# Kernel optimization log

Measured on AMD Instinct MI355X. Metric: run time of the kernel, lower is better.

Reference implementation:

```python
import jax, jax.numpy as jnp
import numpy as np
from jax import lax

F8 = jnp.float8_e4m3fn


def setup_inputs() -> dict:
    key = jax.random.key(0)
    kx, kw = jax.random.split(key)
    x = jax.random.normal(kx, (2, 128, 4, 192, 320), dtype=jnp.float32)
    # matches reset_parameters: normal(0, 0.02) then cast to fp8
    weight = jax.random.normal(kw, (128, 128, 3, 3, 3), dtype=jnp.float32) * 0.02
    return {"x": x, "weight": weight}


def reference(x, weight):
    # fp8 e4m3 quantization round-trip (the torch module stores/consumes fp8),
    # compute/accumulate in fp32 as an fp8 conv kernel would.
    xq = x.astype(F8).astype(jnp.float32)
    wq = weight.astype(F8).astype(jnp.float32)
    # causal temporal padding: (kT-1, 0) = (2, 0); spatial 'same' padding (1,1)
    xp = jnp.pad(xq, ((0, 0), (0, 0), (2, 0), (1, 1), (1, 1)))
    out = lax.conv_general_dilated(
        xp, wq,
        window_strides=(1, 1, 1),
        padding='VALID',
        dimension_numbers=('NCDHW', 'OIDHW', 'NCDHW'),
    )  # (B, 128, 4, 192, 320)
    return out
```

## Files before the change

kernel.cpp:

```cpp
#include <hip/hip_runtime.h>
#include <hip/hip_fp8.h>


using f32x16 = __attribute__((ext_vector_type(16))) float;
using i32x8 = __attribute__((ext_vector_type(8))) int;
typedef long long i64;
struct alignas(16) L2v { i64 x, y; };

namespace {
constexpr int Cc = 128, Dd = 4, Hh = 192, Ww = 320;
constexpr int HP = 194, WP = 322;
constexpr int NTAP = 27;
constexpr size_t PLANE = (size_t)4 * WP * 32;
constexpr size_t XQ_BYTES = (size_t)2 * Dd * HP * PLANE;
constexpr int ZA = 8 * 2 * 2576;
constexpr int ZB = 8 * 192 * 32;
constexpr int GSTR = WP * 32;
}

__global__ __launch_bounds__(256) void zero_pad_kernel(unsigned char* __restrict__ xq) {
  int i = blockIdx.x * 256 + threadIdx.x;
  if (i < ZA) {
    int bd = i / (2 * 2576);
    int r = i - bd * (2 * 2576);
    int hsel = r / 2576, seg = r - hsel * 2576;
    L2v z{0, 0};
    *(L2v*)(xq + ((size_t)bd * HP + (hsel ? 193 : 0)) * PLANE + (size_t)seg * 16) = z;
  } else if (i < ZA + ZB) {
    int j = i - ZA;
    int bd = j / (192 * 32);
    int r = j - bd * (192 * 32);
    int h = r / 32 + 1;
    int t = r & 31;
    int g = t >> 3, s2 = t & 7;
    int wsel = s2 >> 2, part = s2 & 3;
    *(i64*)(xq + ((size_t)bd * HP + h) * PLANE + (size_t)g * GSTR
            + (size_t)(wsel ? 321 : 0) * 32 + part * 8) = 0;
  }
}

__global__ __launch_bounds__(256) void qx_kernel(const float* __restrict__ x,
                                                 unsigned char* __restrict__ xq) {
  __shared__ unsigned char lt[64 * 136];
  const int tid = threadIdx.x;
  const int b = blockIdx.z >> 2, d = blockIdx.z & 3;
  const int h = blockIdx.y;
  const int w0 = blockIdx.x * 64;
  const int wl = tid & 63, cig = tid >> 6;
  const size_t cstr = (size_t)Dd * Hh * Ww;
  const float* xp = x + (((size_t)b * Cc * Dd + d) * Hh + h) * Ww + w0 + wl;
  #pragma unroll 4
  for (int i = 0; i < 32; ++i) {
    int ci = cig * 32 + i;
    __hip_fp8_e4m3 q(xp[ci * cstr]);
    lt[wl * 136 + ci] = q.__x;
  }
  __syncthreads();
  unsigned char* plane = xq + ((size_t)(b * Dd + d) * HP + h + 1) * PLANE;
  {
    int g = tid >> 6, w = tid & 63;
    const unsigned char* src = lt + w * 136 + g * 32;
    i64 a0 = *(const i64*)(src), a1 = *(const i64*)(src + 8);
    i64 a2 = *(const i64*)(src + 16), a3 = *(const i64*)(src + 24);
    unsigned char* dst = plane + (size_t)g * GSTR + (size_t)(w0 + 1 + w) * 32;
    *(L2v*)dst = L2v{a0, a1};
    *(L2v*)(dst + 16) = L2v{a2, a3};
  }
}

__global__ void wpack_kernel(const float* __restrict__ w, unsigned char* __restrict__ wpk) {
  int idx = blockIdx.x * 256 + threadIdx.x;
  if (idx >= Cc * Cc * NTAP) return;
  int tap = idx % NTAP;
  int t = idx / NTAP;
  int ci = t % Cc, co = t / Cc;
  int cc = ci >> 6, ct = co >> 5;
  int lane = (((ci >> 5) & 1) << 5) | (co & 31);
  __hip_fp8_e4m3 q(w[idx]);
  wpk[((((size_t)tap * 2 + cc) * 4 + ct) * 64 + lane) * 32 + (ci & 31)] = q.__x;
}

__global__ __launch_bounds__(256, 3) void conv_mfma(const unsigned char* __restrict__ xq,
                                                    const unsigned char* __restrict__ wpk,
                                                    float* __restrict__ out) {
  __shared__ unsigned char lb[24 * 2112];
  const int tid = threadIdx.x;
  const int lane = tid & 63, wv = tid >> 6;
  const int l31 = lane & 31, chalf = lane >> 5;
  const int hr = wv >> 1, ch = wv & 1;
  const int b = blockIdx.z >> 2, dout = blockIdx.z & 3;
  const int h0 = blockIdx.y * 2;
  const int w0 = blockIdx.x * 64;
  const int kdmin = dout >= 2 ? 0 : 2 - dout;

  f32x16 acc[2][2];
  #pragma unroll
  for (int a = 0; a < 2; ++a)
    #pragma unroll
    for (int n = 0; n < 2; ++n)
      #pragma unroll
      for (int r = 0; r < 16; ++r) acc[a][n][r] = 0.f;

  for (int cc = 0; cc < 2; ++cc) {
    __syncthreads();
    for (int u = tid + kdmin * 528; u < 1584; u += 256) {
      int w = u % 66;
      int rest = u / 66;
      int chf = rest & 1, rest2 = rest >> 1;
      int hrow = rest2 & 3, kd = rest2 >> 2;
      const unsigned char* src = xq
          + ((size_t)(b * Dd + dout + kd - 2) * HP + h0 + hrow) * PLANE
          + (size_t)(cc * 2 + chf) * GSTR + (size_t)(w0 + w) * 32;
      L2v lo = *(const L2v*)src;
      L2v hi = *(const L2v*)(src + 16);
      int t = (w >> 2) & 1;
      unsigned char* base = lb + rest * 2112;
      *(L2v*)(base + (2 * w + t) * 16) = lo;
      *(L2v*)(base + (2 * w + 1 - t) * 16) = hi;
    }
    __syncthreads();
    __builtin_amdgcn_s_setprio(1);
    for (int kd = kdmin; kd < 3; ++kd) {
      #pragma unroll
      for (int kh = 0; kh < 3; ++kh) {
        i32x8 av[3][2];
        #pragma unroll
        for (int kw = 0; kw < 3; ++kw)
          #pragma unroll
          for (int ct = 0; ct < 2; ++ct) {
            const unsigned char* ap = wpk +
                ((((size_t)(kd * 9 + kh * 3 + kw) * 2 + cc) * 4 + ch * 2 + ct) * 64 + lane) * 32;
            int4 alo = *(const int4*)ap;
            int4 ahi = *(const int4*)(ap + 16);
            av[kw][ct][0] = alo.x; av[kw][ct][1] = alo.y;
            av[kw][ct][2] = alo.z; av[kw][ct][3] = alo.w;
            av[kw][ct][4] = ahi.x; av[kw][ct][5] = ahi.y;
            av[kw][ct][6] = ahi.z; av[kw][ct][7] = ahi.w;
          }
        const unsigned char* pbase = lb + (((kd * 4 + hr + kh) * 2 + chalf)) * 2112;
        #pragma unroll
        for (int kw = 0; kw < 3; ++kw)
          #pragma unroll
          for (int nf = 0; nf < 2; ++nf) {
            int wl = nf * 32 + l31 + kw;
            int t = (wl >> 2) & 1;
            int4 blo = *(const int4*)(pbase + (2 * wl + t) * 16);
            int4 bhi = *(const int4*)(pbase + (2 * wl + 1 - t) * 16);
            i32x8 bv;
            bv[0] = blo.x; bv[1] = blo.y; bv[2] = blo.z; bv[3] = blo.w;
            bv[4] = bhi.x; bv[5] = bhi.y; bv[6] = bhi.z; bv[7] = bhi.w;
            #pragma unroll
            for (int ct = 0; ct < 2; ++ct)
              acc[ct][nf] = __builtin_amdgcn_mfma_scale_f32_32x32x64_f8f6f4(
                  av[kw][ct], bv, acc[ct][nf], 0, 0, 0, 127, 0, 127);
          }
      }
    }
    __builtin_amdgcn_s_setprio(0);
  }

  #pragma unroll
  for (int ct = 0; ct < 2; ++ct)
    #pragma unroll
    for (int nf = 0; nf < 2; ++nf) {
      int ww = w0 + nf * 32 + l31;
      #pragma unroll
      for (int reg = 0; reg < 16; ++reg) {
        int co = ch * 64 + ct * 32 + (reg & 3) + 8 * (reg >> 2) + 4 * chalf;
        out[(((size_t)b * Cc + co) * Dd + dout) * (size_t)(Hh * Ww)
            + (size_t)(h0 + hr) * Ww + ww] = acc[ct][nf][reg];
      }
    }
}

extern "C" void kernel_launch(void* const* d_in, const int* in_sizes, int n_in,
                              void* d_out, int out_size, void* d_ws, size_t ws_size,
                              hipStream_t stream) {
  const float* x = (const float*)d_in[0];
  const float* w = (const float*)d_in[1];
  unsigned char* xq = (unsigned char*)d_ws;
  unsigned char* wpk = xq + XQ_BYTES;
  float* out = (float*)d_out;

  int nz = ZA + ZB;
  zero_pad_kernel<<<(nz + 255) / 256, 256, 0, stream>>>(xq);

  dim3 g1(Ww / 64, Hh, 2 * Dd);
  qx_kernel<<<g1, 256, 0, stream>>>(x, xq);

  int nw = Cc * Cc * NTAP;
  wpack_kernel<<<(nw + 255) / 256, 256, 0, stream>>>(w, wpk);

  dim3 g2(Ww / 64, Hh / 2, 2 * Dd);
  conv_mfma<<<g2, 256, 0, stream>>>(xq, wpk, out);
}
```

Baseline: 247.6 us.

## Use 512-thread conv blocks with per-wave 32-channel tiles and XCD-aware swizzle

The conv kernel moves from 256 to 512 threads per block. Each wave now computes one 32-output-channel tile instead of two, so accumulator registers are halved. The loop order changes to iterate over kd in the outer loop, with a smaller per-kd LDS staging buffer, and B-fragment LDS addresses are precomputed once. The grid becomes 1D with an XCD-aware mapping so that neighbouring h-rows share an XCD's L2. The aim is more waves in flight and better L2 locality; the cost is more weight loads per MFMA and more barriers per block.

```diff
diff --git a/kernel.cpp b/kernel.cpp
--- a/kernel.cpp
+++ b/kernel.cpp
@@ -74,103 +74,110 @@
   int tap = idx % NTAP;
   int t = idx / NTAP;
   int ci = t % Cc, co = t / Cc;
-  int cc = ci >> 6, ct = co >> 5;
+  int cc = ci >> 6, cq = co >> 5;
   int lane = (((ci >> 5) & 1) << 5) | (co & 31);
   __hip_fp8_e4m3 q(w[idx]);
-  wpk[((((size_t)tap * 2 + cc) * 4 + ct) * 64 + lane) * 32 + (ci & 31)] = q.__x;
-}
-
-__global__ __launch_bounds__(256, 3) void conv_mfma(const unsigned char* __restrict__ xq,
+  wpk[((((size_t)tap * 2 + cc) * 4 + cq) * 64 + lane) * 32 + (ci & 31)] = q.__x;
+}
+
+__global__ __launch_bounds__(512, 4) void conv_mfma(const unsigned char* __restrict__ xq,
                                                     const unsigned char* __restrict__ wpk,
                                                     float* __restrict__ out) {
-  __shared__ unsigned char lb[24 * 2112];
+  __shared__ unsigned char lb[16 * 2112];
   const int tid = threadIdx.x;
   const int lane = tid & 63, wv = tid >> 6;
   const int l31 = lane & 31, chalf = lane >> 5;
-  const int hr = wv >> 1, ch = wv & 1;
-  const int b = blockIdx.z >> 2, dout = blockIdx.z & 3;
-  const int h0 = blockIdx.y * 2;
-  const int w0 = blockIdx.x * 64;
+  const int hr = wv >> 2, ch = wv & 3;
+  const int id = blockIdx.x;
+  const int xcd = id & 7, j = id >> 3;
+  const int h0l = j / 40, rem = j - h0l * 40;
+  const int z = rem / 5, wx = rem - z * 5;
+  const int b = z >> 2, dout = z & 3;
+  const int h0 = (xcd * 12 + h0l) * 2;
+  const int w0 = wx * 64;
   const int kdmin = dout >= 2 ? 0 : 2 - dout;
 
-  f32x16 acc[2][2];
+  const unsigned char* bbl[3];
+  const unsigned char* bbh[3];
+  {
+    unsigned char* rbase = lb + (hr * 4 + chalf) * 2112;
+    #pragma unroll
+    for (int kw = 0; kw < 3; ++kw) {
+      int wl = l31 + kw;
+      int t = (wl >> 2) & 1;
+      bbl[kw] = rbase + 32 * wl + 16 * t;
+      bbh[kw] = rbase + 32 * wl + 16 * (1 - t);
+    }
+  }
+
+  f32x16 acc[2];
   #pragma unroll
-  for (int a = 0; a < 2; ++a)
-    #pragma unroll
-    for (int n = 0; n < 2; ++n)
-      #pragma unroll
-      for (int r = 0; r < 16; ++r) acc[a][n][r] = 0.f;
-
-  for (int cc = 0; cc < 2; ++cc) {
+  for (int n = 0; n < 2; ++n)
+    #pragma unroll
+    for (int r = 0; r < 16; ++r) acc[n][r] = 0.f;
+
+  for (int kd = kdmin; kd < 3; ++kd) {
     __syncthreads();
-    for (int u = tid + kdmin * 528; u < 1584; u += 256) {
-      int w = u % 66;
-      int rest = u / 66;
-      int chf = rest & 1, rest2 = rest >> 1;
-      int hrow = rest2 & 3, kd = rest2 >> 2;
-      const unsigned char* src = xq
-          + ((size_t)(b * Dd + dout + kd - 2) * HP + h0 + hrow) * PLANE
-          + (size_t)(cc * 2 + chf) * GSTR + (size_t)(w0 + w) * 32;
-      L2v lo = *(const L2v*)src;
-      L2v hi = *(const L2v*)(src + 16);
-      int t = (w >> 2) & 1;
-      unsigned char* base = lb + rest * 2112;
-      *(L2v*)(base + (2 * w + t) * 16) = lo;
-      *(L2v*)(base + (2 * w + 1 - t) * 16) = hi;
+    #pragma unroll
+    for (int it = 0; it < 3; ++it) {
+      int u = tid + it * 512;
+      if (u < 1056) {
+        int w = u % 66, rest = u / 66;
+        int g = rest & 3, hrow = rest >> 2;
+        const unsigned char* src = xq
+            + ((size_t)(b * Dd + dout + kd - 2) * HP + h0 + hrow) * PLANE
+            + (size_t)g * GSTR + (size_t)(w0 + w) * 32;
+        L2v lo = *(const L2v*)src;
+        L2v hi = *(const L2v*)(src + 16);
+        int t = (w >> 2) & 1;
+        unsigned char* base = lb + rest * 2112;
+        *(L2v*)(base + (2 * w + t) * 16) = lo;
+        *(L2v*)(base + (2 * w + 1 - t) * 16) = hi;
+      }
     }
     __syncthreads();
     __builtin_amdgcn_s_setprio(1);
-    for (int kd = kdmin; kd < 3; ++kd) {
+    #pragma unroll
+    for (int kh = 0; kh < 3; ++kh)
       #pragma unroll
-      for (int kh = 0; kh < 3; ++kh) {
-        i32x8 av[3][2];
+      for (int cc = 0; cc < 2; ++cc) {
+        i32x8 av[3];
         #pragma unroll
-        for (int kw = 0; kw < 3; ++kw)
-          #pragma unroll
-          for (int ct = 0; ct < 2; ++ct) {
-            const unsigned char* ap = wpk +
-                ((((size_t)(kd * 9 + kh * 3 + kw) * 2 + cc) * 4 + ch * 2 + ct) * 64 + lane) * 32;
-            int4 alo = *(const int4*)ap;
-            int4 ahi = *(const int4*)(ap + 16);
-            av[kw][ct][0] = alo.x; av[kw][ct][1] = alo.y;
-            av[kw][ct][2] = alo.z; av[kw][ct][3] = alo.w;
-            av[kw][ct][4] = ahi.x; av[kw][ct][5] = ahi.y;
-            av[kw][ct][6] = ahi.z; av[kw][ct][7] = ahi.w;
-          }
-        const unsigned char* pbase = lb + (((kd * 4 + hr + kh) * 2 + chalf)) * 2112;
+        for (int kw = 0; kw < 3; ++kw) {
+          const unsigned char* ap = wpk +
+              ((((size_t)(kd * 9 + kh * 3 + kw) * 2 + cc) * 4 + ch) * 64 + lane) * 32;
+          int4 alo = *(const int4*)ap;
+          int4 ahi = *(const int4*)(ap + 16);
+          av[kw][0] = alo.x; av[kw][1] = alo.y; av[kw][2] = alo.z; av[kw][3] = alo.w;
+          av[kw][4] = ahi.x; av[kw][5] = ahi.y; av[kw][6] = ahi.z; av[kw][7] = ahi.w;
+        }
         #pragma unroll
         for (int kw = 0; kw < 3; ++kw)
           #pragma unroll
           for (int nf = 0; nf < 2; ++nf) {
-            int wl = nf * 32 + l31 + kw;
-            int t = (wl >> 2) & 1;
-            int4 blo = *(const int4*)(pbase + (2 * wl + t) * 16);
-            int4 bhi = *(const int4*)(pbase + (2 * wl + 1 - t) * 16);
+            const int off = (kh * 4 + cc * 2) * 2112 + nf * 1024;
+            int4 blo = *(const int4*)(bbl[kw] + off);
+            int4 bhi = *(const int4*)(bbh[kw] + off);
             i32x8 bv;
             bv[0] = blo.x; bv[1] = blo.y; bv[2] = blo.z; bv[3] = blo.w;
             bv[4] = bhi.x; bv[5] = bhi.y; bv[6] = bhi.z; bv[7] = bhi.w;
-            #pragma unroll
-            for (int ct = 0; ct < 2; ++ct)
-              acc[ct][nf] = __builtin_amdgcn_mfma_scale_f32_32x32x64_f8f6f4(
-                  av[kw][ct], bv, acc[ct][nf], 0, 0, 0, 127, 0, 127);
+            acc[nf] = __builtin_amdgcn_mfma_scale_f32_32x32x64_f8f6f4(
+                av[kw], bv, acc[nf], 0, 0, 0, 127, 0, 127);
           }
       }
+    __builtin_amdgcn_s_setprio(0);
+  }
+
+  #pragma unroll
+  for (int nf = 0; nf < 2; ++nf) {
+    int ww = w0 + nf * 32 + l31;
+    #pragma unroll
+    for (int reg = 0; reg < 16; ++reg) {
+      int co = ch * 32 + (reg & 3) + 8 * (reg >> 2) + 4 * chalf;
+      out[(((size_t)b * Cc + co) * Dd + dout) * (size_t)(Hh * Ww)
+          + (size_t)(h0 + hr) * Ww + ww] = acc[nf][reg];
     }
-    __builtin_amdgcn_s_setprio(0);
-  }
-
-  #pragma unroll
-  for (int ct = 0; ct < 2; ++ct)
-    #pragma unroll
-    for (int nf = 0; nf < 2; ++nf) {
-      int ww = w0 + nf * 32 + l31;
-      #pragma unroll
-      for (int reg = 0; reg < 16; ++reg) {
-        int co = ch * 64 + ct * 32 + (reg & 3) + 8 * (reg >> 2) + 4 * chalf;
-        out[(((size_t)b * Cc + co) * Dd + dout) * (size_t)(Hh * Ww)
-            + (size_t)(h0 + hr) * Ww + ww] = acc[ct][nf][reg];
-      }
-    }
+  }
 }
 
 extern "C" void kernel_launch(void* const* d_in, const int* in_sizes, int n_in,
@@ -191,6 +198,5 @@
   int nw = Cc * Cc * NTAP;
   wpack_kernel<<<(nw + 255) / 256, 256, 0, stream>>>(w, wpk);
 
-  dim3 g2(Ww / 64, Hh / 2, 2 * Dd);
-  conv_mfma<<<g2, 256, 0, stream>>>(xq, wpk, out);
-}
+  conv_mfma<<<dim3(3840), 512, 0, stream>>>(xq, wpk, out);
+}
```

New measurement: 238.4 us. 3.7% less time.
